# Kernel tuning notes

Hardware: AMD Instinct MI355X
Metric: run time of the kernel (lower is better)

The kernel has to match this reference:

```python
import jax, jax.numpy as jnp
import numpy as np

B, S, D = 2, 4096, 1024
H, HD = 16, 64
M = 512              # memseqlen == chunk size
L = 2 * M            # memory + chunk tokens
HID = 2816
EPS = 1e-5


def setup_inputs() -> dict:
    key = jax.random.key(0)
    ks = jax.random.split(key, 16)
    sc = 0.02
    return {
        "x": jax.random.normal(ks[0], (B, S, D), jnp.float32),
        "freqs_cos": jax.random.uniform(ks[1], (L, HD // 2), jnp.float32),
        "freqs_sin": jax.random.uniform(ks[2], (L, HD // 2), jnp.float32),
        "wq": jax.random.normal(ks[3], (D, D), jnp.float32) * sc,
        "wk": jax.random.normal(ks[4], (D, D), jnp.float32) * sc,
        "wv": jax.random.normal(ks[5], (D, D), jnp.float32) * sc,
        "wo": jax.random.normal(ks[6], (D, D), jnp.float32) * sc,
        "wm": jax.random.normal(ks[7], (D, D), jnp.float32) * sc,
        "wkm": jax.random.normal(ks[8], (D, D), jnp.float32) * sc,
        "wvm": jax.random.normal(ks[9], (D, D), jnp.float32) * sc,
        "w1": jax.random.normal(ks[10], (D, HID), jnp.float32) * sc,
        "w3": jax.random.normal(ks[11], (D, HID), jnp.float32) * sc,
        "w2": jax.random.normal(ks[12], (HID, D), jnp.float32) * sc,
        "ffn_norm_w": jnp.ones((D,), jnp.float32),
        "mem_norm_w": jnp.ones((D,), jnp.float32),
        "origin_mem": jnp.zeros((1, M, D), jnp.float32),
    }


def _rmsnorm(x, w):
    return x * jax.lax.rsqrt(jnp.mean(x * x, axis=-1, keepdims=True) + EPS) * w


def _rope(t, cos, sin):
    # t: (B, L, H, HD); cos/sin: (L, HD//2). Adjacent-pair complex rotation (llama2.c style).
    tr = t.reshape(*t.shape[:-1], HD // 2, 2)
    t_r, t_i = tr[..., 0], tr[..., 1]
    c = cos[None, :, None, :]
    s = sin[None, :, None, :]
    o_r = t_r * c - t_i * s
    o_i = t_r * s + t_i * c
    return jnp.stack([o_r, o_i], axis=-1).reshape(t.shape)


def reference(x, freqs_cos, freqs_sin, wq, wk, wv, wo, wm, wkm, wvm,
              w1, w2, w3, ffn_norm_w, mem_norm_w, origin_mem):
    bsz = x.shape[0]
    cos = freqs_cos[:L]
    sin = freqs_sin[:L]
    causal = jnp.tril(jnp.ones((L, L), dtype=bool))
    scale = 1.0 / jnp.sqrt(jnp.asarray(HD, x.dtype))

    def ffn(h):
        return (jax.nn.silu(h @ w1) * (h @ w3)) @ w2

    def step(om, subx):
        # token projections
        xq = (subx @ wq).reshape(bsz, M, H, HD)
        xk = (subx @ wk).reshape(bsz, M, H, HD)
        xv = (subx @ wv).reshape(bsz, M, H, HD)
        # memory glue: wm -> ffn residual -> rmsnorm
        om2 = om @ wm
        om2 = om2 + ffn(_rmsnorm(om2, ffn_norm_w))
        om2 = _rmsnorm(om2, mem_norm_w)
        # memory projections (source bug: mq is overwritten by mk; wqm unused)
        mk = (om2 @ wkm).reshape(bsz, M, H, HD)
        mv = (om2 @ wvm).reshape(bsz, M, H, HD)
        mq = mk
        q = jnp.concatenate([mq, xq], axis=1)  # (B, L, H, HD)
        k = jnp.concatenate([mk, xk], axis=1)
        v = jnp.concatenate([mv, xv], axis=1)
        q = _rope(q, cos, sin)
        k = _rope(k, cos, sin)
        # SDPA, causal over the concatenated length (n_rep == 1, repeat_kv is identity)
        qh = q.transpose(0, 2, 1, 3)
        kh = k.transpose(0, 2, 1, 3)
        vh = v.transpose(0, 2, 1, 3)
        scores = jnp.einsum('bhqd,bhkd->bhqk', qh, kh) * scale
        scores = jnp.where(causal, scores, jnp.finfo(scores.dtype).min)
        attn = jax.nn.softmax(scores, axis=-1)
        out = jnp.einsum('bhqk,bhkd->bhqd', attn, vh)
        out = out.transpose(0, 2, 1, 3).reshape(bsz, L, D)
        om_new = out[:, M:]  # token-part becomes next memory AND this chunk's output
        return om_new, om_new

    om0 = jnp.broadcast_to(origin_mem, (bsz, M, D))
    xc = x.reshape(bsz, S // M, M, D).transpose(1, 0, 2, 3)  # (n_chunks, B, M, D)
    _, outs = jax.lax.scan(step, om0, xc)
    out = outs.transpose(1, 0, 2, 3).reshape(bsz, S, D)
    return out @ wo
```

## Files before the change

kernel.cpp:

```cpp
#include <hip/hip_runtime.h>
#include <hip/hip_bf16.h>


#define D_    1024
#define H_    16
#define HD_   64
#define M_    512
#define L_    1024
#define HID_  2816
#define NSTEP 8

typedef __hip_bfloat16 bf16;
typedef _Float16 f16;
typedef __attribute__((ext_vector_type(8))) short short8;
typedef __attribute__((ext_vector_type(8))) _Float16 f16x8;
typedef __attribute__((ext_vector_type(2))) _Float16 f16x2;
typedef __attribute__((ext_vector_type(4))) float floatx4;

__global__ void probe_dtype(const void* x, int* flag) {
  int lane = threadIdx.x;
  unsigned short v = ((const unsigned short*)x)[2 * lane];
  int e = (v >> 7) & 0xFF;
  bool sane = (e >= 100 && e <= 140);
  unsigned long long m = __ballot(sane);
  if (lane == 0) flag[0] = (__popcll(m) >= 40) ? 1 : 0;
}

__device__ __forceinline__ float load_any(const void* p, long i, int isbf) {
  return isbf ? __bfloat162float(((const bf16*)p)[i]) : ((const float*)p)[i];
}

__global__ __launch_bounds__(256) void transpose_cast(const void* in, bf16* out,
                                                      int K, int N, const int* flagp) {
  __shared__ float tile[32][33];
  int isbf = flagp[0];
  int tx = threadIdx.x & 31, ty = threadIdx.x >> 5;
  int n = blockIdx.x * 32 + tx;
#pragma unroll
  for (int i = 0; i < 4; i++) {
    int k = blockIdx.y * 32 + ty + i * 8;
    tile[ty + i * 8][tx] = load_any(in, (long)k * N + n, isbf);
  }
  __syncthreads();
  int k2 = blockIdx.y * 32 + tx;
#pragma unroll
  for (int i = 0; i < 4; i++) {
    int n2 = blockIdx.x * 32 + ty + i * 8;
    out[(long)n2 * K + k2] = __float2bfloat16(tile[tx][ty + i * 8]);
  }
}

__global__ __launch_bounds__(256) void cast_to_bf16(const void* in, bf16* out, int n,
                                                    const int* flagp) {
  int i = blockIdx.x * 256 + threadIdx.x;
  if (i < n) out[i] = __float2bfloat16(load_any(in, i, flagp[0]));
}

__global__ __launch_bounds__(256) void cast_to_f32(const void* in, float* out, int n,
                                                   const int* flagp) {
  int i = blockIdx.x * 256 + threadIdx.x;
  if (i < n) out[i] = load_any(in, i, flagp[0]);
}

__global__ __launch_bounds__(256) void init_om(const void* in, bf16* om, const int* flagp) {
  int i = blockIdx.x * 256 + threadIdx.x;
  int rem = i & (M_ * D_ - 1);
  om[i] = __float2bfloat16(load_any(in, rem, flagp[0]));
}

__global__ __launch_bounds__(256) void gemm64(
    const bf16* __restrict__ A, const bf16* __restrict__ WT,
    void* __restrict__ out, const int* __restrict__ flagp,
    int N, int K, int out_mode) {
  __shared__ char smem[16384];
  char* aT = smem;
  char* bT = smem + 8192;
  int tid = threadIdx.x;
  int C0 = blockIdx.x * 64, R0 = blockIdx.y * 64;
  int wave = tid >> 6, lane = tid & 63;
  int wm_ = wave >> 1, wn_ = wave & 1;
  floatx4 acc[2][2] = {};

  int q0 = tid, q1 = tid + 256;
  int am0 = q0 >> 3, ac0 = q0 & 7;
  int am1 = q1 >> 3, ac1 = q1 & 7;
  long grow0 = R0 + am0, grow1 = R0 + am1;
  long bn0 = (long)(C0 + am0) * K, bn1 = (long)(C0 + am1) * K;
  int lofa0 = (am0 * 8 + (ac0 ^ (am0 & 7))) * 16;
  int lofa1 = (am1 * 8 + (ac1 ^ (am1 & 7))) * 16;

  for (int k0 = 0; k0 < K; k0 += 64) {
    uint4 va0 = *(const uint4*)(A + grow0 * K + k0 + ac0 * 8);
    uint4 va1 = *(const uint4*)(A + grow1 * K + k0 + ac1 * 8);
    uint4 vb0 = *(const uint4*)(WT + bn0 + k0 + ac0 * 8);
    uint4 vb1 = *(const uint4*)(WT + bn1 + k0 + ac1 * 8);
    __syncthreads();
    *(uint4*)(aT + lofa0) = va0;
    *(uint4*)(aT + lofa1) = va1;
    *(uint4*)(bT + lofa0) = vb0;
    *(uint4*)(bT + lofa1) = vb1;
    __syncthreads();
#pragma unroll
    for (int kki = 0; kki < 2; ++kki) {
      int cbase = kki * 4 + (lane >> 4);
      short8 af[2], bfr[2];
#pragma unroll
      for (int i = 0; i < 2; ++i) {
        int ml = wm_ * 32 + i * 16 + (lane & 15);
        af[i] = *(const short8*)(aT + (ml * 8 + (cbase ^ (ml & 7))) * 16);
        int nl = wn_ * 32 + i * 16 + (lane & 15);
        bfr[i] = *(const short8*)(bT + (nl * 8 + (cbase ^ (nl & 7))) * 16);
      }
#pragma unroll
      for (int i = 0; i < 2; ++i)
#pragma unroll
        for (int j = 0; j < 2; ++j)
          acc[i][j] = __builtin_amdgcn_mfma_f32_16x16x32_bf16(af[i], bfr[j], acc[i][j], 0, 0, 0);
    }
  }
  int isbf = flagp[0];
#pragma unroll
  for (int i = 0; i < 2; ++i)
#pragma unroll
    for (int j = 0; j < 2; ++j) {
      int row = R0 + wm_ * 32 + i * 16 + (lane >> 4) * 4;
      int col = C0 + wn_ * 32 + j * 16 + (lane & 15);
#pragma unroll
      for (int rg = 0; rg < 4; ++rg) {
        float v = acc[i][j][rg];
        long off = (long)(row + rg) * N + col;
        if (out_mode == 0) ((float*)out)[off] = v;
        else if (out_mode == 1) ((f16*)out)[off] = (f16)v;
        else {
          if (isbf) ((bf16*)out)[off] = __float2bfloat16(v);
          else ((float*)out)[off] = v;
        }
      }
    }
}

__global__ __launch_bounds__(256) void gemm128(
    const bf16* __restrict__ A, const bf16* __restrict__ WT,
    void* __restrict__ out, const int* __restrict__ flagp,
    int N, int K, int out_mode) {
  __shared__ char smem[32768];
  int tid = threadIdx.x;
  int w = tid >> 6, lane = tid & 63;
  int C0 = blockIdx.x * 128, R0 = blockIdx.y * 128;
  int wm = (w >> 1) * 64, wn = (w & 1) * 64;
  int g = lane >> 4, n16 = lane & 15;
  floatx4 acc[4][4] = {};
  int lr = lane >> 3, lc = lane & 7;

  for (int k0 = 0; k0 < K; k0 += 64) {
    __syncthreads();
#pragma unroll
    for (int i = 0; i < 4; ++i) {
      int m = w * 32 + i * 8 + lr;
      int cg = lc ^ (m & 7);
      const bf16* ga = A + (size_t)(R0 + m) * K + k0 + cg * 8;
      const bf16* gb = WT + (size_t)(C0 + m) * K + k0 + cg * 8;
      __builtin_amdgcn_global_load_lds(
          (const __attribute__((address_space(1))) void*)ga,
          (__attribute__((address_space(3))) void*)(smem + (w * 32 + i * 8) * 128),
          16, 0, 0);
      __builtin_amdgcn_global_load_lds(
          (const __attribute__((address_space(1))) void*)gb,
          (__attribute__((address_space(3))) void*)(smem + 16384 + (w * 32 + i * 8) * 128),
          16, 0, 0);
    }
    __syncthreads();
#pragma unroll
    for (int kk = 0; kk < 2; ++kk) {
      short8 af[4], bfr[4];
#pragma unroll
      for (int i = 0; i < 4; ++i) {
        int ml = wm + i * 16 + n16;
        af[i] = *(const short8*)(smem + (ml * 8 + ((kk * 4 + g) ^ (ml & 7))) * 16);
        int nl = wn + i * 16 + n16;
        bfr[i] = *(const short8*)(smem + 16384 + (nl * 8 + ((kk * 4 + g) ^ (nl & 7))) * 16);
      }
#pragma unroll
      for (int i = 0; i < 4; ++i)
#pragma unroll
        for (int j = 0; j < 4; ++j)
          acc[i][j] = __builtin_amdgcn_mfma_f32_16x16x32_bf16(af[i], bfr[j], acc[i][j], 0, 0, 0);
    }
  }
  int isbf = flagp[0];
#pragma unroll
  for (int i = 0; i < 4; ++i)
#pragma unroll
    for (int j = 0; j < 4; ++j) {
      int row = R0 + wm + i * 16 + g * 4;
      int col = C0 + wn + j * 16 + n16;
#pragma unroll
      for (int rg = 0; rg < 4; ++rg) {
        float v = acc[i][j][rg];
        long off = (long)(row + rg) * N + col;
        if (out_mode == 0) ((float*)out)[off] = v;
        else if (out_mode == 1) ((f16*)out)[off] = (f16)v;
        else {
          if (isbf) ((bf16*)out)[off] = __float2bfloat16(v);
          else ((float*)out)[off] = v;
        }
      }
    }
}

__global__ __launch_bounds__(256) void rmsnorm_cast(const float* __restrict__ X,
                                                    const float* __restrict__ Wn,
                                                    bf16* __restrict__ Y,
                                                    const float* __restrict__ Xadd) {
  int row = blockIdx.x, tid = threadIdx.x;
  const float* xr = X + (long)row * D_;
  float vals[4], ss = 0.f;
#pragma unroll
  for (int i = 0; i < 4; i++) {
    int c = tid + i * 256;
    float v = xr[c];
    if (Xadd) v += Xadd[(long)row * D_ + c];
    vals[i] = v;
    ss += v * v;
  }
#pragma unroll
  for (int off = 32; off; off >>= 1) ss += __shfl_xor(ss, off);
  __shared__ float wsum[4];
  int wv = tid >> 6, lane = tid & 63;
  if (lane == 0) wsum[wv] = ss;
  __syncthreads();
  ss = wsum[0] + wsum[1] + wsum[2] + wsum[3];
  float r = rsqrtf(ss * (1.0f / D_) + 1e-5f);
#pragma unroll
  for (int i = 0; i < 4; i++) {
    int c = tid + i * 256;
    Y[(long)row * D_ + c] = __float2bfloat16(vals[i] * r * Wn[c]);
  }
}

__global__ __launch_bounds__(256) void silu_mul_cast(const float* __restrict__ g13,
                                                     bf16* __restrict__ u) {
  int c = blockIdx.x * 256 + threadIdx.x;
  int r = blockIdx.y;
  float a = g13[(long)r * (2 * HID_) + c];
  float b = g13[(long)r * (2 * HID_) + HID_ + c];
  float s = a / (1.f + __expf(-a));
  u[(long)r * HID_ + c] = __float2bfloat16(s * b);
}

__global__ __launch_bounds__(256) void rope_x(
    const f16* __restrict__ qkv, const float* __restrict__ cosf,
    const float* __restrict__ sinf, f16* __restrict__ q_x,
    f16* __restrict__ k_x, f16* __restrict__ v_xT) {
  __shared__ f16 tile[64][72];
  int pt = blockIdx.x;
  int t = blockIdx.y;
  int bh = blockIdx.z;
  int b = bh >> 4, h = bh & 15;
  int tid = threadIdx.x;
  int i = tid & 31, p0 = tid >> 5;
  size_t slab = (size_t)t * 32 + bh;
#pragma unroll
  for (int j = 0; j < 8; ++j) {
    int pl = p0 + j * 8;
    int m = pt * 64 + pl;
    int pos = 512 + m;
    long base = ((long)b * 4096 + t * 512 + m) * 3072 + h * 64 + 2 * i;
    float c = cosf[pos * 32 + i], s = sinf[pos * 32 + i];
    float q0 = (float)qkv[base], q1 = (float)qkv[base + 1];
    f16x2 qw; qw.x = (f16)((q0 * c - q1 * s) * 0.125f);
    qw.y = (f16)((q0 * s + q1 * c) * 0.125f);
    *(f16x2*)(q_x + (slab * 512 + m) * 64 + 2 * i) = qw;
    float k0 = (float)qkv[base + 1024], k1 = (float)qkv[base + 1025];
    f16x2 kw; kw.x = (f16)(k0 * c - k1 * s); kw.y = (f16)(k0 * s + k1 * c);
    *(f16x2*)(k_x + (slab * 512 + m) * 64 + 2 * i) = kw;
    tile[2 * i][pl] = qkv[base + 2048];
    tile[2 * i + 1][pl] = qkv[base + 2049];
  }
  __syncthreads();
#pragma unroll
  for (int j = 0; j < 8; ++j) {
    int d = p0 + j * 8;
    f16x2 vv; vv.x = tile[d][2 * i]; vv.y = tile[d][2 * i + 1];
    *(f16x2*)(v_xT + (slab * 64 + d) * 512 + pt * 64 + 2 * i) = vv;
  }
}

__global__ __launch_bounds__(256) void rope_mem(
    const f16* __restrict__ mkv, const float* __restrict__ cosf,
    const float* __restrict__ sinf, f16* __restrict__ k_mem,
    f16* __restrict__ v_memT) {
  __shared__ f16 tile[64][72];
  int pt = blockIdx.x;
  int bh = blockIdx.y;
  int b = bh >> 4, h = bh & 15;
  int tid = threadIdx.x;
  int i = tid & 31, p0 = tid >> 5;
#pragma unroll
  for (int j = 0; j < 8; ++j) {
    int pl = p0 + j * 8;
    int pos = pt * 64 + pl;
    long base = ((long)(b * 512 + pos)) * 2048 + h * 64 + 2 * i;
    float c = cosf[pos * 32 + i], s = sinf[pos * 32 + i];
    float k0 = (float)mkv[base], k1 = (float)mkv[base + 1];
    f16x2 kw; kw.x = (f16)(k0 * c - k1 * s); kw.y = (f16)(k0 * s + k1 * c);
    *(f16x2*)(k_mem + ((size_t)bh * 512 + pos) * 64 + 2 * i) = kw;
    tile[2 * i][pl] = mkv[base + 1024];
    tile[2 * i + 1][pl] = mkv[base + 1025];
  }
  __syncthreads();
#pragma unroll
  for (int j = 0; j < 8; ++j) {
    int d = p0 + j * 8;
    f16x2 vv; vv.x = tile[d][2 * i]; vv.y = tile[d][2 * i + 1];
    *(f16x2*)(v_memT + ((size_t)bh * 64 + d) * 512 + pt * 64 + 2 * i) = vv;
  }
}

__global__ __launch_bounds__(256) void attn_mfma(
    const f16* __restrict__ q_x, const f16* __restrict__ k_mem,
    const f16* __restrict__ v_memT, const f16* __restrict__ k_x,
    const f16* __restrict__ v_xT, bf16* __restrict__ om_bf,
    bf16* __restrict__ outs_bf, int t) {
  __shared__ char smem[24576];
  int qt = blockIdx.x, bh = blockIdx.y;
  int tid = threadIdx.x;
  int w = tid >> 6, lane = tid & 63;
  int g = lane >> 4, n16 = lane & 15;
  int numc = 9 + qt;
  int pos = 512 + qt * 64 + w * 16 + n16;
  size_t slab = (size_t)t * 32 + bh;

  f16x8 qf[2];
  {
    const f16* qp = q_x + (slab * 512 + qt * 64 + w * 16 + n16) * 64 + g * 8;
    qf[0] = *(const f16x8*)(qp);
    qf[1] = *(const f16x8*)(qp + 32);
  }
  floatx4 O[4] = {};
  float mrun = -1e30f, lrun = 0.f;

  int id0 = tid, id1 = tid + 256;
  int r0 = id0 >> 3, c0 = id0 & 7;
  int r1 = id1 >> 3, c1 = id1 & 7;
  int lof0 = ((r0 << 3) | (c0 ^ (r0 & 7))) * 16;
  int lof1 = ((r1 << 3) | (c1 ^ (r1 & 7))) * 16;

  auto kaddr = [&](int c, int r) -> const f16* {
    return (c < 8) ? k_mem + ((size_t)bh * 512 + c * 64 + r) * 64
                   : k_x + (slab * 512 + (c - 8) * 64 + r) * 64;
  };
  auto vaddr = [&](int c, int d) -> const f16* {
    return (c < 8) ? v_memT + ((size_t)bh * 64 + d) * 512 + c * 64
                   : v_xT + (slab * 64 + d) * 512 + (c - 8) * 64;
  };

  uint4 kv0 = *(const uint4*)(kaddr(0, r0) + c0 * 8);
  uint4 kv1 = *(const uint4*)(kaddr(0, r1) + c1 * 8);
  uint4 vv0 = *(const uint4*)(vaddr(0, r0) + c0 * 8);
  uint4 vv1 = *(const uint4*)(vaddr(0, r1) + c1 * 8);

  char* Pw = smem + 16384 + w * 2048;

  for (int c = 0; c < numc; ++c) {
    __syncthreads();
    *(uint4*)(smem + lof0) = kv0;
    *(uint4*)(smem + lof1) = kv1;
    *(uint4*)(smem + 8192 + lof0) = vv0;
    *(uint4*)(smem + 8192 + lof1) = vv1;
    if (c + 1 < numc) {
      kv0 = *(const uint4*)(kaddr(c + 1, r0) + c0 * 8);
      kv1 = *(const uint4*)(kaddr(c + 1, r1) + c1 * 8);
      vv0 = *(const uint4*)(vaddr(c + 1, r0) + c0 * 8);
      vv1 = *(const uint4*)(vaddr(c + 1, r1) + c1 * 8);
    }
    __syncthreads();

    floatx4 S[4] = {};
#pragma unroll
    for (int kk = 0; kk < 2; ++kk) {
#pragma unroll
      for (int tn = 0; tn < 4; ++tn) {
        int row = tn * 16 + n16;
        f16x8 kf = *(const f16x8*)(smem + (((row << 3) | ((kk * 4 + g) ^ (row & 7))) * 16));
        S[tn] = __builtin_amdgcn_mfma_f32_16x16x32_f16(kf, qf[kk], S[tn], 0, 0, 0);
      }
    }
    if (c == numc - 1) {
      int kb = 512 + (c - 8) * 64;
#pragma unroll
      for (int tn = 0; tn < 4; ++tn)
#pragma unroll
        for (int r = 0; r < 4; ++r) {
          int key = kb + tn * 16 + g * 4 + r;
          if (key > pos) S[tn][r] = -1e30f;
        }
    }
    float smax = -1e30f;
#pragma unroll
    for (int tn = 0; tn < 4; ++tn)
#pragma unroll
      for (int r = 0; r < 4; ++r) smax = fmaxf(smax, S[tn][r]);
    smax = fmaxf(smax, __shfl_xor(smax, 16));
    smax = fmaxf(smax, __shfl_xor(smax, 32));
    float newm = fmaxf(mrun, smax);
    float corr = __expf(mrun - newm);
    mrun = newm;
    float lsum = 0.f;
    f16 pv[16];
#pragma unroll
    for (int tn = 0; tn < 4; ++tn)
#pragma unroll
      for (int r = 0; r < 4; ++r) {
        float p = __expf(S[tn][r] - newm);
        lsum += p;
        pv[tn * 4 + r] = (f16)p;
      }
    lsum += __shfl_xor(lsum, 16);
    lsum += __shfl_xor(lsum, 32);
    lrun = lrun * corr + lsum;
    float cr[4];
#pragma unroll
    for (int r = 0; r < 4; ++r) cr[r] = __shfl(corr, g * 4 + r);
#pragma unroll
    for (int dt = 0; dt < 4; ++dt)
#pragma unroll
      for (int r = 0; r < 4; ++r) O[dt][r] *= cr[r];
#pragma unroll
    for (int tn = 0; tn < 4; ++tn)
#pragma unroll
      for (int r = 0; r < 4; ++r) {
        int kap = tn * 16 + g * 4 + r;
        *(f16*)(Pw + (((n16 << 3) | ((kap >> 3) ^ (n16 & 7))) * 16 + (kap & 7) * 2)) =
            pv[tn * 4 + r];
      }
#pragma unroll
    for (int kk = 0; kk < 2; ++kk) {
      f16x8 pf = *(const f16x8*)(Pw + (((n16 << 3) | ((kk * 4 + g) ^ (n16 & 7))) * 16));
#pragma unroll
      for (int dt = 0; dt < 4; ++dt) {
        int row = dt * 16 + n16;
        f16x8 vf =
            *(const f16x8*)(smem + 8192 + (((row << 3) | ((kk * 4 + g) ^ (row & 7))) * 16));
        O[dt] = __builtin_amdgcn_mfma_f32_16x16x32_f16(pf, vf, O[dt], 0, 0, 0);
      }
    }
  }
  float rl = 1.0f / lrun;
  float rlr[4];
#pragma unroll
  for (int r = 0; r < 4; ++r) rlr[r] = __shfl(rl, g * 4 + r);
  int b = bh >> 4, h = bh & 15;
#pragma unroll
  for (int dt = 0; dt < 4; ++dt)
#pragma unroll
    for (int r = 0; r < 4; ++r) {
      int qq = qt * 64 + w * 16 + g * 4 + r;
      bf16 v = __float2bfloat16(O[dt][r] * rlr[r]);
      size_t col = h * 64 + dt * 16 + n16;
      om_bf[((size_t)(b * 512 + qq)) * 1024 + col] = v;
      outs_bf[((size_t)(b * 4096 + t * 512 + qq)) * 1024 + col] = v;
    }
}

extern "C" void kernel_launch(void* const* d_in, const int* in_sizes, int n_in,
                              void* d_out, int out_size, void* d_ws, size_t ws_size,
                              hipStream_t stream) {
  (void)in_sizes; (void)n_in; (void)out_size; (void)ws_size;
  const void* x   = d_in[0];
  const void* fc  = d_in[1];
  const void* fs  = d_in[2];
  const void* wq  = d_in[3];
  const void* wk  = d_in[4];
  const void* wv  = d_in[5];
  const void* wo  = d_in[6];
  const void* wm  = d_in[7];
  const void* wkm = d_in[8];
  const void* wvm = d_in[9];
  const void* w1  = d_in[10];
  const void* w3  = d_in[11];
  const void* w2  = d_in[12];
  const void* fnw = d_in[13];
  const void* mnw = d_in[14];
  const void* om0 = d_in[15];

  char* p = (char*)d_ws;
  auto alloc = [&](size_t bytes) -> char* {
    char* r = p;
    p += (bytes + 255) & ~(size_t)255;
    return r;
  };
  int*   flag    = (int*)alloc(256);
  bf16*  wqkvT   = (bf16*)alloc((size_t)3 * 1048576 * 2);
  bf16*  wmT     = (bf16*)alloc((size_t)1048576 * 2);
  bf16*  wkmvmT  = (bf16*)alloc((size_t)2 * 1048576 * 2);
  bf16*  w13T    = (bf16*)alloc((size_t)2 * 2883584 * 2);
  bf16*  w2T     = (bf16*)alloc((size_t)2883584 * 2);
  bf16*  woT     = (bf16*)alloc((size_t)1048576 * 2);
  bf16*  xb      = (bf16*)alloc((size_t)8388608 * 2);
  float* cosf    = (float*)alloc((size_t)32768 * 4);
  float* sinf    = (float*)alloc((size_t)32768 * 4);
  float* ffnw    = (float*)alloc((size_t)1024 * 4);
  float* memw    = (float*)alloc((size_t)1024 * 4);
  bf16*  om_bf   = (bf16*)alloc((size_t)1048576 * 2);
  bf16*  outs_bf = (bf16*)alloc((size_t)8388608 * 2);
  f16*   q_x     = (f16*)alloc((size_t)8 * 32 * 512 * 64 * 2);
  f16*   k_x     = (f16*)alloc((size_t)8 * 32 * 512 * 64 * 2);
  f16*   v_xT    = (f16*)alloc((size_t)8 * 32 * 512 * 64 * 2);
  char*  shr     = alloc((size_t)8192 * 3072 * 2);
  f16*   qkvf_all = (f16*)shr;
  char*  lp = shr;
  auto lalloc = [&](size_t bytes) -> char* {
    char* r = lp;
    lp += (bytes + 255) & ~(size_t)255;
    return r;
  };
  float* om2a   = (float*)lalloc((size_t)1048576 * 4);
  bf16*  h_bf   = (bf16*)lalloc((size_t)1048576 * 2);
  float* g13    = (float*)lalloc((size_t)5767168 * 4);
  bf16*  u_bf   = (bf16*)lalloc((size_t)2883584 * 2);
  float* fbuf   = (float*)lalloc((size_t)1048576 * 4);
  bf16*  om2_bf = (bf16*)lalloc((size_t)1048576 * 2);
  f16*   mkv    = (f16*)lalloc((size_t)2097152 * 2);
  f16*   k_mem  = (f16*)lalloc((size_t)1048576 * 2);
  f16*   v_memT = (f16*)lalloc((size_t)1048576 * 2);

  dim3 tb(256);
  probe_dtype<<<1, 64, 0, stream>>>(x, flag);

  transpose_cast<<<dim3(32, 32), tb, 0, stream>>>(wq, wqkvT, 1024, 1024, flag);
  transpose_cast<<<dim3(32, 32), tb, 0, stream>>>(wk, wqkvT + 1048576, 1024, 1024, flag);
  transpose_cast<<<dim3(32, 32), tb, 0, stream>>>(wv, wqkvT + 2 * 1048576, 1024, 1024, flag);
  transpose_cast<<<dim3(32, 32), tb, 0, stream>>>(wm, wmT, 1024, 1024, flag);
  transpose_cast<<<dim3(32, 32), tb, 0, stream>>>(wkm, wkmvmT, 1024, 1024, flag);
  transpose_cast<<<dim3(32, 32), tb, 0, stream>>>(wvm, wkmvmT + 1048576, 1024, 1024, flag);
  transpose_cast<<<dim3(88, 32), tb, 0, stream>>>(w1, w13T, 1024, 2816, flag);
  transpose_cast<<<dim3(88, 32), tb, 0, stream>>>(w3, w13T + 2883584, 1024, 2816, flag);
  transpose_cast<<<dim3(32, 88), tb, 0, stream>>>(w2, w2T, 2816, 1024, flag);
  transpose_cast<<<dim3(32, 32), tb, 0, stream>>>(wo, woT, 1024, 1024, flag);

  cast_to_bf16<<<32768, tb, 0, stream>>>(x, xb, 8388608, flag);
  cast_to_f32<<<128, tb, 0, stream>>>(fc, cosf, 32768, flag);
  cast_to_f32<<<128, tb, 0, stream>>>(fs, sinf, 32768, flag);
  cast_to_f32<<<4, tb, 0, stream>>>(fnw, ffnw, 1024, flag);
  cast_to_f32<<<4, tb, 0, stream>>>(mnw, memw, 1024, flag);
  init_om<<<4096, tb, 0, stream>>>(om0, om_bf, flag);

  gemm128<<<dim3(24, 64), tb, 0, stream>>>(xb, wqkvT, qkvf_all, flag, 3072, 1024, 1);
  rope_x<<<dim3(8, 8, 32), tb, 0, stream>>>(qkvf_all, cosf, sinf, q_x, k_x, v_xT);

  for (int t = 0; t < NSTEP; ++t) {
    gemm64<<<dim3(16, 16), tb, 0, stream>>>(om_bf, wmT, om2a, flag, 1024, 1024, 0);
    rmsnorm_cast<<<1024, tb, 0, stream>>>(om2a, ffnw, h_bf, nullptr);
    gemm128<<<dim3(44, 8), tb, 0, stream>>>(h_bf, w13T, g13, flag, 5632, 1024, 0);
    silu_mul_cast<<<dim3(11, 1024), tb, 0, stream>>>(g13, u_bf);
    gemm64<<<dim3(16, 16), tb, 0, stream>>>(u_bf, w2T, fbuf, flag, 1024, 2816, 0);
    rmsnorm_cast<<<1024, tb, 0, stream>>>(om2a, memw, om2_bf, fbuf);
    gemm64<<<dim3(32, 16), tb, 0, stream>>>(om2_bf, wkmvmT, mkv, flag, 2048, 1024, 1);
    rope_mem<<<dim3(8, 32), tb, 0, stream>>>(mkv, cosf, sinf, k_mem, v_memT);
    attn_mfma<<<dim3(8, 32), tb, 0, stream>>>(q_x, k_mem, v_memT, k_x, v_xT,
                                              om_bf, outs_bf, t);
  }
  gemm128<<<dim3(8, 64), tb, 0, stream>>>(outs_bf, woT, d_out, flag, 1024, 1024, 2);
}
```

Baseline: 1.270 ms.

## Fuse scan loop into one persistent kernel with grid barriers and folded norms

```diff
diff --git a/kernel.cpp b/kernel.cpp
--- a/kernel.cpp
+++ b/kernel.cpp
@@ -2,12 +2,6 @@
 #include <hip/hip_bf16.h>
 
 
-#define D_    1024
-#define H_    16
-#define HD_   64
-#define M_    512
-#define L_    1024
-#define HID_  2816
 #define NSTEP 8
 
 typedef __hip_bfloat16 bf16;
@@ -30,113 +24,56 @@
   return isbf ? __bfloat162float(((const bf16*)p)[i]) : ((const float*)p)[i];
 }
 
-__global__ __launch_bounds__(256) void transpose_cast(const void* in, bf16* out,
-                                                      int K, int N, const int* flagp) {
+struct TArg { const void* src; const void* scl; bf16* dst; int K, N, start; };
+struct TArgs { TArg a[10]; };
+
+__global__ __launch_bounds__(256) void transpose_all(TArgs ta, const int* flagp) {
   __shared__ float tile[32][33];
   int isbf = flagp[0];
+  int bid = blockIdx.x;
+  int z = 0;
+  while (z < 9 && bid >= ta.a[z + 1].start) ++z;
+  const TArg& e = ta.a[z];
+  int local = bid - e.start;
+  int tnx = e.N >> 5;
+  int bx = local % tnx, by = local / tnx;
   int tx = threadIdx.x & 31, ty = threadIdx.x >> 5;
-  int n = blockIdx.x * 32 + tx;
+  int n = bx * 32 + tx;
 #pragma unroll
   for (int i = 0; i < 4; i++) {
-    int k = blockIdx.y * 32 + ty + i * 8;
-    tile[ty + i * 8][tx] = load_any(in, (long)k * N + n, isbf);
+    int k = by * 32 + ty + i * 8;
+    tile[ty + i * 8][tx] = load_any(e.src, (long)k * e.N + n, isbf);
   }
   __syncthreads();
-  int k2 = blockIdx.y * 32 + tx;
+  int k2 = by * 32 + tx;
+  float s = e.scl ? load_any(e.scl, k2, isbf) : 1.f;
 #pragma unroll
   for (int i = 0; i < 4; i++) {
-    int n2 = blockIdx.x * 32 + ty + i * 8;
-    out[(long)n2 * K + k2] = __float2bfloat16(tile[tx][ty + i * 8]);
+    int n2 = bx * 32 + ty + i * 8;
+    e.dst[(long)n2 * e.K + k2] = __float2bfloat16(tile[tx][ty + i * 8] * s);
   }
 }
 
-__global__ __launch_bounds__(256) void cast_to_bf16(const void* in, bf16* out, int n,
-                                                    const int* flagp) {
-  int i = blockIdx.x * 256 + threadIdx.x;
-  if (i < n) out[i] = __float2bfloat16(load_any(in, i, flagp[0]));
-}
-
-__global__ __launch_bounds__(256) void cast_to_f32(const void* in, float* out, int n,
-                                                   const int* flagp) {
-  int i = blockIdx.x * 256 + threadIdx.x;
-  if (i < n) out[i] = load_any(in, i, flagp[0]);
-}
-
-__global__ __launch_bounds__(256) void init_om(const void* in, bf16* om, const int* flagp) {
-  int i = blockIdx.x * 256 + threadIdx.x;
-  int rem = i & (M_ * D_ - 1);
-  om[i] = __float2bfloat16(load_any(in, rem, flagp[0]));
-}
-
-__global__ __launch_bounds__(256) void gemm64(
-    const bf16* __restrict__ A, const bf16* __restrict__ WT,
-    void* __restrict__ out, const int* __restrict__ flagp,
-    int N, int K, int out_mode) {
-  __shared__ char smem[16384];
-  char* aT = smem;
-  char* bT = smem + 8192;
-  int tid = threadIdx.x;
-  int C0 = blockIdx.x * 64, R0 = blockIdx.y * 64;
-  int wave = tid >> 6, lane = tid & 63;
-  int wm_ = wave >> 1, wn_ = wave & 1;
-  floatx4 acc[2][2] = {};
-
-  int q0 = tid, q1 = tid + 256;
-  int am0 = q0 >> 3, ac0 = q0 & 7;
-  int am1 = q1 >> 3, ac1 = q1 & 7;
-  long grow0 = R0 + am0, grow1 = R0 + am1;
-  long bn0 = (long)(C0 + am0) * K, bn1 = (long)(C0 + am1) * K;
-  int lofa0 = (am0 * 8 + (ac0 ^ (am0 & 7))) * 16;
-  int lofa1 = (am1 * 8 + (ac1 ^ (am1 & 7))) * 16;
-
-  for (int k0 = 0; k0 < K; k0 += 64) {
-    uint4 va0 = *(const uint4*)(A + grow0 * K + k0 + ac0 * 8);
-    uint4 va1 = *(const uint4*)(A + grow1 * K + k0 + ac1 * 8);
-    uint4 vb0 = *(const uint4*)(WT + bn0 + k0 + ac0 * 8);
-    uint4 vb1 = *(const uint4*)(WT + bn1 + k0 + ac1 * 8);
-    __syncthreads();
-    *(uint4*)(aT + lofa0) = va0;
-    *(uint4*)(aT + lofa1) = va1;
-    *(uint4*)(bT + lofa0) = vb0;
-    *(uint4*)(bT + lofa1) = vb1;
-    __syncthreads();
-#pragma unroll
-    for (int kki = 0; kki < 2; ++kki) {
-      int cbase = kki * 4 + (lane >> 4);
-      short8 af[2], bfr[2];
-#pragma unroll
-      for (int i = 0; i < 2; ++i) {
-        int ml = wm_ * 32 + i * 16 + (lane & 15);
-        af[i] = *(const short8*)(aT + (ml * 8 + (cbase ^ (ml & 7))) * 16);
-        int nl = wn_ * 32 + i * 16 + (lane & 15);
-        bfr[i] = *(const short8*)(bT + (nl * 8 + (cbase ^ (nl & 7))) * 16);
-      }
-#pragma unroll
-      for (int i = 0; i < 2; ++i)
-#pragma unroll
-        for (int j = 0; j < 2; ++j)
-          acc[i][j] = __builtin_amdgcn_mfma_f32_16x16x32_bf16(af[i], bfr[j], acc[i][j], 0, 0, 0);
-    }
-  }
+__global__ __launch_bounds__(256) void prep(const void* x, const void* fc,
+                                            const void* fs, const void* om0,
+                                            bf16* xb, float* cosf, float* sinf,
+                                            bf16* om_bf, float* rs1, float* rs2,
+                                            int* bar, const int* flagp) {
+  long idx = (long)blockIdx.x * 256 + threadIdx.x;
   int isbf = flagp[0];
-#pragma unroll
-  for (int i = 0; i < 2; ++i)
-#pragma unroll
-    for (int j = 0; j < 2; ++j) {
-      int row = R0 + wm_ * 32 + i * 16 + (lane >> 4) * 4;
-      int col = C0 + wn_ * 32 + j * 16 + (lane & 15);
-#pragma unroll
-      for (int rg = 0; rg < 4; ++rg) {
-        float v = acc[i][j][rg];
-        long off = (long)(row + rg) * N + col;
-        if (out_mode == 0) ((float*)out)[off] = v;
-        else if (out_mode == 1) ((f16*)out)[off] = (f16)v;
-        else {
-          if (isbf) ((bf16*)out)[off] = __float2bfloat16(v);
-          else ((float*)out)[off] = v;
-        }
-      }
-    }
+  if (idx < 8388608) { xb[idx] = __float2bfloat16(load_any(x, idx, isbf)); return; }
+  long i = idx - 8388608;
+  if (i < 32768) { cosf[i] = load_any(fc, i, isbf); return; }
+  i -= 32768;
+  if (i < 32768) { sinf[i] = load_any(fs, i, isbf); return; }
+  i -= 32768;
+  if (i < 1048576) { om_bf[i] = __float2bfloat16(load_any(om0, i & 524287, isbf)); return; }
+  i -= 1048576;
+  if (i < 1024) { rs1[i] = 0.f; return; }
+  i -= 1024;
+  if (i < 1024) { rs2[i] = 0.f; return; }
+  i -= 1024;
+  if (i < 128) bar[i] = 0;
 }
 
 __global__ __launch_bounds__(256) void gemm128(
@@ -206,46 +143,6 @@
         }
       }
     }
-}
-
-__global__ __launch_bounds__(256) void rmsnorm_cast(const float* __restrict__ X,
-                                                    const float* __restrict__ Wn,
-                                                    bf16* __restrict__ Y,
-                                                    const float* __restrict__ Xadd) {
-  int row = blockIdx.x, tid = threadIdx.x;
-  const float* xr = X + (long)row * D_;
-  float vals[4], ss = 0.f;
-#pragma unroll
-  for (int i = 0; i < 4; i++) {
-    int c = tid + i * 256;
-    float v = xr[c];
-    if (Xadd) v += Xadd[(long)row * D_ + c];
-    vals[i] = v;
-    ss += v * v;
-  }
-#pragma unroll
-  for (int off = 32; off; off >>= 1) ss += __shfl_xor(ss, off);
-  __shared__ float wsum[4];
-  int wv = tid >> 6, lane = tid & 63;
-  if (lane == 0) wsum[wv] = ss;
-  __syncthreads();
-  ss = wsum[0] + wsum[1] + wsum[2] + wsum[3];
-  float r = rsqrtf(ss * (1.0f / D_) + 1e-5f);
-#pragma unroll
-  for (int i = 0; i < 4; i++) {
-    int c = tid + i * 256;
-    Y[(long)row * D_ + c] = __float2bfloat16(vals[i] * r * Wn[c]);
-  }
-}
-
-__global__ __launch_bounds__(256) void silu_mul_cast(const float* __restrict__ g13,
-                                                     bf16* __restrict__ u) {
-  int c = blockIdx.x * 256 + threadIdx.x;
-  int r = blockIdx.y;
-  float a = g13[(long)r * (2 * HID_) + c];
-  float b = g13[(long)r * (2 * HID_) + HID_ + c];
-  float s = a / (1.f + __expf(-a));
-  u[(long)r * HID_ + c] = __float2bfloat16(s * b);
 }
 
 __global__ __launch_bounds__(256) void rope_x(
@@ -286,181 +183,489 @@
   }
 }
 
-__global__ __launch_bounds__(256) void rope_mem(
-    const f16* __restrict__ mkv, const float* __restrict__ cosf,
-    const float* __restrict__ sinf, f16* __restrict__ k_mem,
-    f16* __restrict__ v_memT) {
-  __shared__ f16 tile[64][72];
-  int pt = blockIdx.x;
-  int bh = blockIdx.y;
-  int b = bh >> 4, h = bh & 15;
-  int tid = threadIdx.x;
-  int i = tid & 31, p0 = tid >> 5;
-#pragma unroll
-  for (int j = 0; j < 8; ++j) {
-    int pl = p0 + j * 8;
-    int pos = pt * 64 + pl;
-    long base = ((long)(b * 512 + pos)) * 2048 + h * 64 + 2 * i;
-    float c = cosf[pos * 32 + i], s = sinf[pos * 32 + i];
-    float k0 = (float)mkv[base], k1 = (float)mkv[base + 1];
-    f16x2 kw; kw.x = (f16)(k0 * c - k1 * s); kw.y = (f16)(k0 * s + k1 * c);
-    *(f16x2*)(k_mem + ((size_t)bh * 512 + pos) * 64 + 2 * i) = kw;
-    tile[2 * i][pl] = mkv[base + 1024];
-    tile[2 * i + 1][pl] = mkv[base + 1025];
+#define NBLK 256
+__device__ __forceinline__ void gbar(int* bar) {
+  __syncthreads();
+  if (threadIdx.x == 0) {
+    __threadfence();
+    int* cnt = bar;
+    int* gen = bar + 64;
+    int g = __hip_atomic_load(gen, __ATOMIC_RELAXED, __HIP_MEMORY_SCOPE_AGENT);
+    int old = __hip_atomic_fetch_add(cnt, 1, __ATOMIC_ACQ_REL, __HIP_MEMORY_SCOPE_AGENT);
+    if (old == NBLK - 1) {
+      __hip_atomic_store(cnt, 0, __ATOMIC_RELAXED, __HIP_MEMORY_SCOPE_AGENT);
+      __hip_atomic_fetch_add(gen, 1, __ATOMIC_ACQ_REL, __HIP_MEMORY_SCOPE_AGENT);
+    } else {
+      while (__hip_atomic_load(gen, __ATOMIC_ACQUIRE, __HIP_MEMORY_SCOPE_AGENT) == g)
+        __builtin_amdgcn_s_sleep(2);
+    }
+    __threadfence();
   }
   __syncthreads();
-#pragma unroll
-  for (int j = 0; j < 8; ++j) {
-    int d = p0 + j * 8;
-    f16x2 vv; vv.x = tile[d][2 * i]; vv.y = tile[d][2 * i + 1];
-    *(f16x2*)(v_memT + ((size_t)bh * 64 + d) * 512 + pt * 64 + 2 * i) = vv;
-  }
-}
-
-__global__ __launch_bounds__(256) void attn_mfma(
-    const f16* __restrict__ q_x, const f16* __restrict__ k_mem,
-    const f16* __restrict__ v_memT, const f16* __restrict__ k_x,
-    const f16* __restrict__ v_xT, bf16* __restrict__ om_bf,
-    bf16* __restrict__ outs_bf, int t) {
-  __shared__ char smem[24576];
-  int qt = blockIdx.x, bh = blockIdx.y;
-  int tid = threadIdx.x;
+}
+
+__global__ __launch_bounds__(256) void scan_loop(
+    const bf16* __restrict__ wmT, const bf16* __restrict__ w13T,
+    const bf16* __restrict__ w2T, const bf16* __restrict__ wkmvmT,
+    const f16* __restrict__ q_x, const f16* __restrict__ k_x,
+    const f16* __restrict__ v_xT, const float* __restrict__ cosf,
+    const float* __restrict__ sinf, bf16* __restrict__ om_bf,
+    bf16* __restrict__ outs_bf, float* __restrict__ om2a,
+    float* __restrict__ g13, float* __restrict__ om2b,
+    f16* __restrict__ mkv, float* __restrict__ rs1, float* __restrict__ rs2,
+    int* __restrict__ bar) {
+  __shared__ char smem[32768];
+  int bid = blockIdx.x, tid = threadIdx.x;
   int w = tid >> 6, lane = tid & 63;
   int g = lane >> 4, n16 = lane & 15;
-  int numc = 9 + qt;
-  int pos = 512 + qt * 64 + w * 16 + n16;
-  size_t slab = (size_t)t * 32 + bh;
-
-  f16x8 qf[2];
-  {
-    const f16* qp = q_x + (slab * 512 + qt * 64 + w * 16 + n16) * 64 + g * 8;
-    qf[0] = *(const f16x8*)(qp);
-    qf[1] = *(const f16x8*)(qp + 32);
+  int wm_ = w >> 1, wn_ = w & 1;
+
+  for (int t = 0; t < NSTEP; ++t) {
+    {
+      int C0 = (bid & 15) * 64, R0 = (bid >> 4) * 64;
+      floatx4 acc[2][2] = {};
+      int am0 = tid >> 3, ac0 = tid & 7;
+      int am1 = (tid + 256) >> 3, ac1 = tid & 7;
+      long grow0 = R0 + am0, grow1 = R0 + am1;
+      long bn0 = (long)(C0 + am0) * 1024, bn1 = (long)(C0 + am1) * 1024;
+      int lofa0 = (am0 * 8 + (ac0 ^ (am0 & 7))) * 16;
+      int lofa1 = (am1 * 8 + (ac1 ^ (am1 & 7))) * 16;
+      for (int k0 = 0; k0 < 1024; k0 += 64) {
+        uint4 va0 = *(const uint4*)(om_bf + grow0 * 1024 + k0 + ac0 * 8);
+        uint4 va1 = *(const uint4*)(om_bf + grow1 * 1024 + k0 + ac1 * 8);
+        uint4 vb0 = *(const uint4*)(wmT + bn0 + k0 + ac0 * 8);
+        uint4 vb1 = *(const uint4*)(wmT + bn1 + k0 + ac1 * 8);
+        __syncthreads();
+        *(uint4*)(smem + lofa0) = va0;
+        *(uint4*)(smem + lofa1) = va1;
+        *(uint4*)(smem + 8192 + lofa0) = vb0;
+        *(uint4*)(smem + 8192 + lofa1) = vb1;
+        __syncthreads();
+#pragma unroll
+        for (int kki = 0; kki < 2; ++kki) {
+          int cb = kki * 4 + g;
+          short8 af[2], bfr[2];
+#pragma unroll
+          for (int i = 0; i < 2; ++i) {
+            int ml = wm_ * 32 + i * 16 + n16;
+            af[i] = *(const short8*)(smem + (ml * 8 + (cb ^ (ml & 7))) * 16);
+            int nl = wn_ * 32 + i * 16 + n16;
+            bfr[i] = *(const short8*)(smem + 8192 + (nl * 8 + (cb ^ (nl & 7))) * 16);
+          }
+#pragma unroll
+          for (int i = 0; i < 2; ++i)
+#pragma unroll
+            for (int j = 0; j < 2; ++j)
+              acc[i][j] = __builtin_amdgcn_mfma_f32_16x16x32_bf16(af[i], bfr[j], acc[i][j], 0, 0, 0);
+        }
+      }
+      __syncthreads();
+      float* rsl = (float*)(smem + 16384);
+      if (tid < 64) rsl[tid] = 0.f;
+      __syncthreads();
+#pragma unroll
+      for (int i = 0; i < 2; ++i)
+#pragma unroll
+        for (int rg = 0; rg < 4; ++rg) {
+          int rl = wm_ * 32 + i * 16 + g * 4 + rg;
+          float sq = 0.f;
+#pragma unroll
+          for (int j = 0; j < 2; ++j) {
+            float v = acc[i][j][rg];
+            sq += v * v;
+            om2a[(long)(R0 + rl) * 1024 + C0 + wn_ * 32 + j * 16 + n16] = v;
+          }
+          atomicAdd(&rsl[rl], sq);
+        }
+      __syncthreads();
+      if (tid < 64) atomicAdd(&rs1[R0 + tid], rsl[tid]);
+    }
+    gbar(bar);
+
+    for (int tile = bid; tile < 352; tile += NBLK) {
+      int C0 = (tile % 44) * 128, R0 = (tile / 44) * 128;
+      int wmm = (w >> 1) * 64, wnn = (w & 1) * 64;
+      floatx4 acc[4][4] = {};
+      int lr = lane >> 3, lc = lane & 7;
+      int ams[4], acs[4];
+      float sca[4];
+#pragma unroll
+      for (int i = 0; i < 4; ++i) {
+        int id = tid + 256 * i;
+        ams[i] = id >> 3;
+        acs[i] = id & 7;
+        sca[i] = rsqrtf(rs1[R0 + ams[i]] * (1.f / 1024.f) + 1e-5f);
+      }
+      for (int k0 = 0; k0 < 1024; k0 += 64) {
+        uint4 av[4];
+#pragma unroll
+        for (int i = 0; i < 4; ++i) {
+          const float* ap = om2a + (size_t)(R0 + ams[i]) * 1024 + k0 + acs[i] * 8;
+          float4 x0 = *(const float4*)ap, x1 = *(const float4*)(ap + 4);
+          union { bf16 b[8]; uint4 u; } pk;
+          pk.b[0] = __float2bfloat16(x0.x * sca[i]);
+          pk.b[1] = __float2bfloat16(x0.y * sca[i]);
+          pk.b[2] = __float2bfloat16(x0.z * sca[i]);
+          pk.b[3] = __float2bfloat16(x0.w * sca[i]);
+          pk.b[4] = __float2bfloat16(x1.x * sca[i]);
+          pk.b[5] = __float2bfloat16(x1.y * sca[i]);
+          pk.b[6] = __float2bfloat16(x1.z * sca[i]);
+          pk.b[7] = __float2bfloat16(x1.w * sca[i]);
+          av[i] = pk.u;
+        }
+        __syncthreads();
+#pragma unroll
+        for (int i = 0; i < 4; ++i)
+          *(uint4*)(smem + (ams[i] * 8 + (acs[i] ^ (ams[i] & 7))) * 16) = av[i];
+#pragma unroll
+        for (int i = 0; i < 4; ++i) {
+          int m = w * 32 + i * 8 + lr;
+          int cg = lc ^ (m & 7);
+          const bf16* gb = w13T + (size_t)(C0 + m) * 1024 + k0 + cg * 8;
+          __builtin_amdgcn_global_load_lds(
+              (const __attribute__((address_space(1))) void*)gb,
+              (__attribute__((address_space(3))) void*)(smem + 16384 + (w * 32 + i * 8) * 128),
+              16, 0, 0);
+        }
+        __syncthreads();
+#pragma unroll
+        for (int kk = 0; kk < 2; ++kk) {
+          short8 af[4], bfr[4];
+#pragma unroll
+          for (int i = 0; i < 4; ++i) {
+            int ml = wmm + i * 16 + n16;
+            af[i] = *(const short8*)(smem + (ml * 8 + ((kk * 4 + g) ^ (ml & 7))) * 16);
+            int nl = wnn + i * 16 + n16;
+            bfr[i] = *(const short8*)(smem + 16384 + (nl * 8 + ((kk * 4 + g) ^ (nl & 7))) * 16);
+          }
+#pragma unroll
+          for (int i = 0; i < 4; ++i)
+#pragma unroll
+            for (int j = 0; j < 4; ++j)
+              acc[i][j] = __builtin_amdgcn_mfma_f32_16x16x32_bf16(af[i], bfr[j], acc[i][j], 0, 0, 0);
+        }
+      }
+#pragma unroll
+      for (int i = 0; i < 4; ++i)
+#pragma unroll
+        for (int j = 0; j < 4; ++j) {
+          int row = R0 + wmm + i * 16 + g * 4;
+          int col = C0 + wnn + j * 16 + n16;
+#pragma unroll
+          for (int rg = 0; rg < 4; ++rg)
+            g13[(long)(row + rg) * 5632 + col] = acc[i][j][rg];
+        }
+      __syncthreads();
+    }
+    gbar(bar);
+
+    {
+      int C0 = (bid & 15) * 64, R0 = (bid >> 4) * 64;
+      floatx4 acc[2][2] = {};
+      int am0 = tid >> 3, ac0 = tid & 7;
+      int am1 = (tid + 256) >> 3, ac1 = tid & 7;
+      long bn0 = (long)(C0 + am0) * 2816, bn1 = (long)(C0 + am1) * 2816;
+      int lofa0 = (am0 * 8 + (ac0 ^ (am0 & 7))) * 16;
+      int lofa1 = (am1 * 8 + (ac1 ^ (am1 & 7))) * 16;
+      for (int k0 = 0; k0 < 2816; k0 += 64) {
+        uint4 va[2];
+        int amv[2] = {am0, am1}, acv[2] = {ac0, ac1};
+#pragma unroll
+        for (int i = 0; i < 2; ++i) {
+          const float* g1p = g13 + (size_t)(R0 + amv[i]) * 5632 + k0 + acv[i] * 8;
+          const float* g3p = g1p + 2816;
+          float4 a0 = *(const float4*)g1p, a1 = *(const float4*)(g1p + 4);
+          float4 b0 = *(const float4*)g3p, b1 = *(const float4*)(g3p + 4);
+          union { bf16 b[8]; uint4 u; } pk;
+          pk.b[0] = __float2bfloat16(a0.x / (1.f + __expf(-a0.x)) * b0.x);
+          pk.b[1] = __float2bfloat16(a0.y / (1.f + __expf(-a0.y)) * b0.y);
+          pk.b[2] = __float2bfloat16(a0.z / (1.f + __expf(-a0.z)) * b0.z);
+          pk.b[3] = __float2bfloat16(a0.w / (1.f + __expf(-a0.w)) * b0.w);
+          pk.b[4] = __float2bfloat16(a1.x / (1.f + __expf(-a1.x)) * b1.x);
+          pk.b[5] = __float2bfloat16(a1.y / (1.f + __expf(-a1.y)) * b1.y);
+          pk.b[6] = __float2bfloat16(a1.z / (1.f + __expf(-a1.z)) * b1.z);
+          pk.b[7] = __float2bfloat16(a1.w / (1.f + __expf(-a1.w)) * b1.w);
+          va[i] = pk.u;
+        }
+        uint4 vb0 = *(const uint4*)(w2T + bn0 + k0 + ac0 * 8);
+        uint4 vb1 = *(const uint4*)(w2T + bn1 + k0 + ac1 * 8);
+        __syncthreads();
+        *(uint4*)(smem + lofa0) = va[0];
+        *(uint4*)(smem + lofa1) = va[1];
+        *(uint4*)(smem + 8192 + lofa0) = vb0;
+        *(uint4*)(smem + 8192 + lofa1) = vb1;
+        __syncthreads();
+#pragma unroll
+        for (int kki = 0; kki < 2; ++kki) {
+          int cb = kki * 4 + g;
+          short8 af[2], bfr[2];
+#pragma unroll
+          for (int i = 0; i < 2; ++i) {
+            int ml = wm_ * 32 + i * 16 + n16;
+            af[i] = *(const short8*)(smem + (ml * 8 + (cb ^ (ml & 7))) * 16);
+            int nl = wn_ * 32 + i * 16 + n16;
+            bfr[i] = *(const short8*)(smem + 8192 + (nl * 8 + (cb ^ (nl & 7))) * 16);
+          }
+#pragma unroll
+          for (int i = 0; i < 2; ++i)
+#pragma unroll
+            for (int j = 0; j < 2; ++j)
+              acc[i][j] = __builtin_amdgcn_mfma_f32_16x16x32_bf16(af[i], bfr[j], acc[i][j], 0, 0, 0);
+        }
+      }
+      __syncthreads();
+      float* rsl = (float*)(smem + 16384);
+      if (tid < 64) rsl[tid] = 0.f;
+      __syncthreads();
+#pragma unroll
+      for (int i = 0; i < 2; ++i)
+#pragma unroll
+        for (int rg = 0; rg < 4; ++rg) {
+          int rl = wm_ * 32 + i * 16 + g * 4 + rg;
+          float sq = 0.f;
+#pragma unroll
+          for (int j = 0; j < 2; ++j) {
+            long off = (long)(R0 + rl) * 1024 + C0 + wn_ * 32 + j * 16 + n16;
+            float o2 = om2a[off] + acc[i][j][rg];
+            om2b[off] = o2;
+            sq += o2 * o2;
+          }
+          atomicAdd(&rsl[rl], sq);
+        }
+      __syncthreads();
+      if (tid < 64) atomicAdd(&rs2[R0 + tid], rsl[tid]);
+    }
+    gbar(bar);
+
+#pragma unroll
+    for (int half = 0; half < 2; ++half) {
+      int tile = bid + half * NBLK;
+      int C0 = (tile & 31) * 64, R0 = (tile >> 5) * 64;
+      floatx4 acc[2][2] = {};
+      int am0 = tid >> 3, ac0 = tid & 7;
+      int am1 = (tid + 256) >> 3, ac1 = tid & 7;
+      long bn0 = (long)(C0 + am0) * 1024, bn1 = (long)(C0 + am1) * 1024;
+      int lofa0 = (am0 * 8 + (ac0 ^ (am0 & 7))) * 16;
+      int lofa1 = (am1 * 8 + (ac1 ^ (am1 & 7))) * 16;
+      float sc0 = rsqrtf(rs2[R0 + am0] * (1.f / 1024.f) + 1e-5f);
+      float sc1 = rsqrtf(rs2[R0 + am1] * (1.f / 1024.f) + 1e-5f);
+      for (int k0 = 0; k0 < 1024; k0 += 64) {
+        uint4 va[2];
+        int amv[2] = {am0, am1}, acv[2] = {ac0, ac1};
+        float scv[2] = {sc0, sc1};
+#pragma unroll
+        for (int i = 0; i < 2; ++i) {
+          const float* ap = om2b + (size_t)(R0 + amv[i]) * 1024 + k0 + acv[i] * 8;
+          float4 x0 = *(const float4*)ap, x1 = *(const float4*)(ap + 4);
+          union { bf16 b[8]; uint4 u; } pk;
+          pk.b[0] = __float2bfloat16(x0.x * scv[i]);
+          pk.b[1] = __float2bfloat16(x0.y * scv[i]);
+          pk.b[2] = __float2bfloat16(x0.z * scv[i]);
+          pk.b[3] = __float2bfloat16(x0.w * scv[i]);
+          pk.b[4] = __float2bfloat16(x1.x * scv[i]);
+          pk.b[5] = __float2bfloat16(x1.y * scv[i]);
+          pk.b[6] = __float2bfloat16(x1.z * scv[i]);
+          pk.b[7] = __float2bfloat16(x1.w * scv[i]);
+          va[i] = pk.u;
+        }
+        uint4 vb0 = *(const uint4*)(wkmvmT + bn0 + k0 + ac0 * 8);
+        uint4 vb1 = *(const uint4*)(wkmvmT + bn1 + k0 + ac1 * 8);
+        __syncthreads();
+        *(uint4*)(smem + lofa0) = va[0];
+        *(uint4*)(smem + lofa1) = va[1];
+        *(uint4*)(smem + 8192 + lofa0) = vb0;
+        *(uint4*)(smem + 8192 + lofa1) = vb1;
+        __syncthreads();
+#pragma unroll
+        for (int kki = 0; kki < 2; ++kki) {
+          int cb = kki * 4 + g;
+          short8 af[2], bfr[2];
+#pragma unroll
+          for (int i = 0; i < 2; ++i) {
+            int ml = wm_ * 32 + i * 16 + n16;
+            af[i] = *(const short8*)(smem + (ml * 8 + (cb ^ (ml & 7))) * 16);
+            int nl = wn_ * 32 + i * 16 + n16;
+            bfr[i] = *(const short8*)(smem + 8192 + (nl * 8 + (cb ^ (nl & 7))) * 16);
+          }
+#pragma unroll
+          for (int i = 0; i < 2; ++i)
+#pragma unroll
+            for (int j = 0; j < 2; ++j)
+              acc[i][j] = __builtin_amdgcn_mfma_f32_16x16x32_bf16(af[i], bfr[j], acc[i][j], 0, 0, 0);
+        }
+      }
+#pragma unroll
+      for (int i = 0; i < 2; ++i)
+#pragma unroll
+        for (int j = 0; j < 2; ++j) {
+          int row = R0 + wm_ * 32 + i * 16 + g * 4;
+          int col = C0 + wn_ * 32 + j * 16 + n16;
+#pragma unroll
+          for (int rg = 0; rg < 4; ++rg)
+            mkv[(long)(row + rg) * 2048 + col] = (f16)acc[i][j][rg];
+        }
+      __syncthreads();
+    }
+    gbar(bar);
+
+    {
+      if (bid == 0) {
+        rs1[tid] = 0.f; rs1[tid + 256] = 0.f; rs1[tid + 512] = 0.f; rs1[tid + 768] = 0.f;
+      } else if (bid == 1) {
+        rs2[tid] = 0.f; rs2[tid + 256] = 0.f; rs2[tid + 512] = 0.f; rs2[tid + 768] = 0.f;
+      }
+      int qt = bid & 7, bh = bid >> 3;
+      int batb = bh >> 4, hh = bh & 15;
+      int numc = 9 + qt;
+      int pos = 512 + qt * 64 + w * 16 + n16;
+      size_t slab = (size_t)t * 32 + bh;
+      f16x8 qf[2];
+      {
+        const f16* qp = q_x + (slab * 512 + qt * 64 + w * 16 + n16) * 64 + g * 8;
+        qf[0] = *(const f16x8*)(qp);
+        qf[1] = *(const f16x8*)(qp + 32);
+      }
+      floatx4 O[4] = {};
+      float mrun = -1e30f, lrun = 0.f;
+      int r0 = tid >> 3, c0 = tid & 7;
+      int r1 = (tid + 256) >> 3, c1 = tid & 7;
+      int lof0 = ((r0 << 3) | (c0 ^ (r0 & 7))) * 16;
+      int lof1 = ((r1 << 3) | (c1 ^ (r1 & 7))) * 16;
+
+      auto ld_k = [&](int c, int r, int dc) -> uint4 {
+        union { f16x8 h; uint4 u; } cv;
+        if (c < 8) {
+          int pp = c * 64 + r;
+          f16x8 kv = *(const f16x8*)(mkv + ((size_t)(batb * 512 + pp)) * 2048 + hh * 64 + dc * 8);
+#pragma unroll
+          for (int j = 0; j < 4; ++j) {
+            float cs = cosf[pp * 32 + dc * 4 + j], sn = sinf[pp * 32 + dc * 4 + j];
+            float a = (float)kv[2 * j], bq = (float)kv[2 * j + 1];
+            cv.h[2 * j] = (f16)(a * cs - bq * sn);
+            cv.h[2 * j + 1] = (f16)(a * sn + bq * cs);
+          }
+        } else {
+          cv.u = *(const uint4*)(k_x + (slab * 512 + (c - 8) * 64 + r) * 64 + dc * 8);
+        }
+        return cv.u;
+      };
+      auto ld_v = [&](int c, int r, int dc) -> uint4 {
+        union { f16x8 h; uint4 u; } cv;
+        if (c < 8) {
+#pragma unroll
+          for (int j = 0; j < 8; ++j)
+            cv.h[j] = mkv[((size_t)(batb * 512 + c * 64 + dc * 8 + j)) * 2048 + 1024 + hh * 64 + r];
+        } else {
+          cv.u = *(const uint4*)(v_xT + (slab * 64 + r) * 512 + (c - 8) * 64 + dc * 8);
+        }
+        return cv.u;
+      };
+
+      uint4 kv0 = ld_k(0, r0, c0), kv1 = ld_k(0, r1, c1);
+      uint4 vv0 = ld_v(0, r0, c0), vv1 = ld_v(0, r1, c1);
+      char* Pw = smem + 16384 + w * 2048;
+
+      for (int c = 0; c < numc; ++c) {
+        __syncthreads();
+        *(uint4*)(smem + lof0) = kv0;
+        *(uint4*)(smem + lof1) = kv1;
+        *(uint4*)(smem + 8192 + lof0) = vv0;
+        *(uint4*)(smem + 8192 + lof1) = vv1;
+        if (c + 1 < numc) {
+          kv0 = ld_k(c + 1, r0, c0);
+          kv1 = ld_k(c + 1, r1, c1);
+          vv0 = ld_v(c + 1, r0, c0);
+          vv1 = ld_v(c + 1, r1, c1);
+        }
+        __syncthreads();
+
+        floatx4 S[4] = {};
+#pragma unroll
+        for (int kk = 0; kk < 2; ++kk) {
+#pragma unroll
+          for (int tn = 0; tn < 4; ++tn) {
+            int row = tn * 16 + n16;
+            f16x8 kf = *(const f16x8*)(smem + (((row << 3) | ((kk * 4 + g) ^ (row & 7))) * 16));
+            S[tn] = __builtin_amdgcn_mfma_f32_16x16x32_f16(kf, qf[kk], S[tn], 0, 0, 0);
+          }
+        }
+        if (c == numc - 1) {
+          int kb = 512 + (c - 8) * 64;
+#pragma unroll
+          for (int tn = 0; tn < 4; ++tn)
+#pragma unroll
+            for (int r = 0; r < 4; ++r) {
+              int key = kb + tn * 16 + g * 4 + r;
+              if (key > pos) S[tn][r] = -1e30f;
+            }
+        }
+        float smax = -1e30f;
+#pragma unroll
+        for (int tn = 0; tn < 4; ++tn)
+#pragma unroll
+          for (int r = 0; r < 4; ++r) smax = fmaxf(smax, S[tn][r]);
+        smax = fmaxf(smax, __shfl_xor(smax, 16));
+        smax = fmaxf(smax, __shfl_xor(smax, 32));
+        float newm = fmaxf(mrun, smax);
+        float corr = __expf(mrun - newm);
+        mrun = newm;
+        float lsum = 0.f;
+        f16 pv[16];
+#pragma unroll
+        for (int tn = 0; tn < 4; ++tn)
+#pragma unroll
+          for (int r = 0; r < 4; ++r) {
+            float p = __expf(S[tn][r] - newm);
+            lsum += p;
+            pv[tn * 4 + r] = (f16)p;
+          }
+        lsum += __shfl_xor(lsum, 16);
+        lsum += __shfl_xor(lsum, 32);
+        lrun = lrun * corr + lsum;
+        float cr[4];
+#pragma unroll
+        for (int r = 0; r < 4; ++r) cr[r] = __shfl(corr, g * 4 + r);
+#pragma unroll
+        for (int dt = 0; dt < 4; ++dt)
+#pragma unroll
+          for (int r = 0; r < 4; ++r) O[dt][r] *= cr[r];
+#pragma unroll
+        for (int tn = 0; tn < 4; ++tn)
+#pragma unroll
+          for (int r = 0; r < 4; ++r) {
+            int kap = tn * 16 + g * 4 + r;
+            *(f16*)(Pw + (((n16 << 3) | ((kap >> 3) ^ (n16 & 7))) * 16 + (kap & 7) * 2)) =
+                pv[tn * 4 + r];
+          }
+#pragma unroll
+        for (int kk = 0; kk < 2; ++kk) {
+          f16x8 pf = *(const f16x8*)(Pw + (((n16 << 3) | ((kk * 4 + g) ^ (n16 & 7))) * 16));
+#pragma unroll
+          for (int dt = 0; dt < 4; ++dt) {
+            int row = dt * 16 + n16;
+            f16x8 vf =
+                *(const f16x8*)(smem + 8192 + (((row << 3) | ((kk * 4 + g) ^ (row & 7))) * 16));
+            O[dt] = __builtin_amdgcn_mfma_f32_16x16x32_f16(pf, vf, O[dt], 0, 0, 0);
+          }
+        }
+      }
+      float rl = 1.0f / lrun;
+      float rlr[4];
+#pragma unroll
+      for (int r = 0; r < 4; ++r) rlr[r] = __shfl(rl, g * 4 + r);
+#pragma unroll
+      for (int dt = 0; dt < 4; ++dt)
+#pragma unroll
+        for (int r = 0; r < 4; ++r) {
+          int qq = qt * 64 + w * 16 + g * 4 + r;
+          bf16 v = __float2bfloat16(O[dt][r] * rlr[r]);
+          size_t col = hh * 64 + dt * 16 + n16;
+          om_bf[((size_t)(batb * 512 + qq)) * 1024 + col] = v;
+          outs_bf[((size_t)(batb * 4096 + t * 512 + qq)) * 1024 + col] = v;
+        }
+    }
+    gbar(bar);
   }
-  floatx4 O[4] = {};
-  float mrun = -1e30f, lrun = 0.f;
-
-  int id0 = tid, id1 = tid + 256;
-  int r0 = id0 >> 3, c0 = id0 & 7;
-  int r1 = id1 >> 3, c1 = id1 & 7;
-  int lof0 = ((r0 << 3) | (c0 ^ (r0 & 7))) * 16;
-  int lof1 = ((r1 << 3) | (c1 ^ (r1 & 7))) * 16;
-
-  auto kaddr = [&](int c, int r) -> const f16* {
-    return (c < 8) ? k_mem + ((size_t)bh * 512 + c * 64 + r) * 64
-                   : k_x + (slab * 512 + (c - 8) * 64 + r) * 64;
-  };
-  auto vaddr = [&](int c, int d) -> const f16* {
-    return (c < 8) ? v_memT + ((size_t)bh * 64 + d) * 512 + c * 64
-                   : v_xT + (slab * 64 + d) * 512 + (c - 8) * 64;
-  };
-
-  uint4 kv0 = *(const uint4*)(kaddr(0, r0) + c0 * 8);
-  uint4 kv1 = *(const uint4*)(kaddr(0, r1) + c1 * 8);
-  uint4 vv0 = *(const uint4*)(vaddr(0, r0) + c0 * 8);
-  uint4 vv1 = *(const uint4*)(vaddr(0, r1) + c1 * 8);
-
-  char* Pw = smem + 16384 + w * 2048;
-
-  for (int c = 0; c < numc; ++c) {
-    __syncthreads();
-    *(uint4*)(smem + lof0) = kv0;
-    *(uint4*)(smem + lof1) = kv1;
-    *(uint4*)(smem + 8192 + lof0) = vv0;
-    *(uint4*)(smem + 8192 + lof1) = vv1;
-    if (c + 1 < numc) {
-      kv0 = *(const uint4*)(kaddr(c + 1, r0) + c0 * 8);
-      kv1 = *(const uint4*)(kaddr(c + 1, r1) + c1 * 8);
-      vv0 = *(const uint4*)(vaddr(c + 1, r0) + c0 * 8);
-      vv1 = *(const uint4*)(vaddr(c + 1, r1) + c1 * 8);
-    }
-    __syncthreads();
-
-    floatx4 S[4] = {};
-#pragma unroll
-    for (int kk = 0; kk < 2; ++kk) {
-#pragma unroll
-      for (int tn = 0; tn < 4; ++tn) {
-        int row = tn * 16 + n16;
-        f16x8 kf = *(const f16x8*)(smem + (((row << 3) | ((kk * 4 + g) ^ (row & 7))) * 16));
-        S[tn] = __builtin_amdgcn_mfma_f32_16x16x32_f16(kf, qf[kk], S[tn], 0, 0, 0);
-      }
-    }
-    if (c == numc - 1) {
-      int kb = 512 + (c - 8) * 64;
-#pragma unroll
-      for (int tn = 0; tn < 4; ++tn)
-#pragma unroll
-        for (int r = 0; r < 4; ++r) {
-          int key = kb + tn * 16 + g * 4 + r;
-          if (key > pos) S[tn][r] = -1e30f;
-        }
-    }
-    float smax = -1e30f;
-#pragma unroll
-    for (int tn = 0; tn < 4; ++tn)
-#pragma unroll
-      for (int r = 0; r < 4; ++r) smax = fmaxf(smax, S[tn][r]);
-    smax = fmaxf(smax, __shfl_xor(smax, 16));
-    smax = fmaxf(smax, __shfl_xor(smax, 32));
-    float newm = fmaxf(mrun, smax);
-    float corr = __expf(mrun - newm);
-    mrun = newm;
-    float lsum = 0.f;
-    f16 pv[16];
-#pragma unroll
-    for (int tn = 0; tn < 4; ++tn)
-#pragma unroll
-      for (int r = 0; r < 4; ++r) {
-        float p = __expf(S[tn][r] - newm);
-        lsum += p;
-        pv[tn * 4 + r] = (f16)p;
-      }
-    lsum += __shfl_xor(lsum, 16);
-    lsum += __shfl_xor(lsum, 32);
-    lrun = lrun * corr + lsum;
-    float cr[4];
-#pragma unroll
-    for (int r = 0; r < 4; ++r) cr[r] = __shfl(corr, g * 4 + r);
-#pragma unroll
-    for (int dt = 0; dt < 4; ++dt)
-#pragma unroll
-      for (int r = 0; r < 4; ++r) O[dt][r] *= cr[r];
-#pragma unroll
-    for (int tn = 0; tn < 4; ++tn)
-#pragma unroll
-      for (int r = 0; r < 4; ++r) {
-        int kap = tn * 16 + g * 4 + r;
-        *(f16*)(Pw + (((n16 << 3) | ((kap >> 3) ^ (n16 & 7))) * 16 + (kap & 7) * 2)) =
-            pv[tn * 4 + r];
-      }
-#pragma unroll
-    for (int kk = 0; kk < 2; ++kk) {
-      f16x8 pf = *(const f16x8*)(Pw + (((n16 << 3) | ((kk * 4 + g) ^ (n16 & 7))) * 16));
-#pragma unroll
-      for (int dt = 0; dt < 4; ++dt) {
-        int row = dt * 16 + n16;
-        f16x8 vf =
-            *(const f16x8*)(smem + 8192 + (((row << 3) | ((kk * 4 + g) ^ (row & 7))) * 16));
-        O[dt] = __builtin_amdgcn_mfma_f32_16x16x32_f16(pf, vf, O[dt], 0, 0, 0);
-      }
-    }
-  }
-  float rl = 1.0f / lrun;
-  float rlr[4];
-#pragma unroll
-  for (int r = 0; r < 4; ++r) rlr[r] = __shfl(rl, g * 4 + r);
-  int b = bh >> 4, h = bh & 15;
-#pragma unroll
-  for (int dt = 0; dt < 4; ++dt)
-#pragma unroll
-    for (int r = 0; r < 4; ++r) {
-      int qq = qt * 64 + w * 16 + g * 4 + r;
-      bf16 v = __float2bfloat16(O[dt][r] * rlr[r]);
-      size_t col = h * 64 + dt * 16 + n16;
-      om_bf[((size_t)(b * 512 + qq)) * 1024 + col] = v;
-      outs_bf[((size_t)(b * 4096 + t * 512 + qq)) * 1024 + col] = v;
-    }
 }
 
 extern "C" void kernel_launch(void* const* d_in, const int* in_sizes, int n_in,
@@ -491,6 +696,7 @@
     return r;
   };
   int*   flag    = (int*)alloc(256);
+  int*   bar     = (int*)alloc(512);
   bf16*  wqkvT   = (bf16*)alloc((size_t)3 * 1048576 * 2);
   bf16*  wmT     = (bf16*)alloc((size_t)1048576 * 2);
   bf16*  wkmvmT  = (bf16*)alloc((size_t)2 * 1048576 * 2);
@@ -500,13 +706,13 @@
   bf16*  xb      = (bf16*)alloc((size_t)8388608 * 2);
   float* cosf    = (float*)alloc((size_t)32768 * 4);
   float* sinf    = (float*)alloc((size_t)32768 * 4);
-  float* ffnw    = (float*)alloc((size_t)1024 * 4);
-  float* memw    = (float*)alloc((size_t)1024 * 4);
   bf16*  om_bf   = (bf16*)alloc((size_t)1048576 * 2);
   bf16*  outs_bf = (bf16*)alloc((size_t)8388608 * 2);
   f16*   q_x     = (f16*)alloc((size_t)8 * 32 * 512 * 64 * 2);
   f16*   k_x     = (f16*)alloc((size_t)8 * 32 * 512 * 64 * 2);
   f16*   v_xT    = (f16*)alloc((size_t)8 * 32 * 512 * 64 * 2);
+  float* rs1     = (float*)alloc((size_t)1024 * 4);
+  float* rs2     = (float*)alloc((size_t)1024 * 4);
   char*  shr     = alloc((size_t)8192 * 3072 * 2);
   f16*   qkvf_all = (f16*)shr;
   char*  lp = shr;
@@ -515,51 +721,42 @@
     lp += (bytes + 255) & ~(size_t)255;
     return r;
   };
-  float* om2a   = (float*)lalloc((size_t)1048576 * 4);
-  bf16*  h_bf   = (bf16*)lalloc((size_t)1048576 * 2);
-  float* g13    = (float*)lalloc((size_t)5767168 * 4);
-  bf16*  u_bf   = (bf16*)lalloc((size_t)2883584 * 2);
-  float* fbuf   = (float*)lalloc((size_t)1048576 * 4);
-  bf16*  om2_bf = (bf16*)lalloc((size_t)1048576 * 2);
-  f16*   mkv    = (f16*)lalloc((size_t)2097152 * 2);
-  f16*   k_mem  = (f16*)lalloc((size_t)1048576 * 2);
-  f16*   v_memT = (f16*)lalloc((size_t)1048576 * 2);
+  float* om2a = (float*)lalloc((size_t)1048576 * 4);
+  float* g13  = (float*)lalloc((size_t)5767168 * 4);
+  float* om2b = (float*)lalloc((size_t)1048576 * 4);
+  f16*   mkv  = (f16*)lalloc((size_t)2097152 * 2);
 
   dim3 tb(256);
   probe_dtype<<<1, 64, 0, stream>>>(x, flag);
 
-  transpose_cast<<<dim3(32, 32), tb, 0, stream>>>(wq, wqkvT, 1024, 1024, flag);
-  transpose_cast<<<dim3(32, 32), tb, 0, stream>>>(wk, wqkvT + 1048576, 1024, 1024, flag);
-  transpose_cast<<<dim3(32, 32), tb, 0, stream>>>(wv, wqkvT + 2 * 1048576, 1024, 1024, flag);
-  transpose_cast<<<dim3(32, 32), tb, 0, stream>>>(wm, wmT, 1024, 1024, flag);
-  transpose_cast<<<dim3(32, 32), tb, 0, stream>>>(wkm, wkmvmT, 1024, 1024, flag);
-  transpose_cast<<<dim3(32, 32), tb, 0, stream>>>(wvm, wkmvmT + 1048576, 1024, 1024, flag);
-  transpose_cast<<<dim3(88, 32), tb, 0, stream>>>(w1, w13T, 1024, 2816, flag);
-  transpose_cast<<<dim3(88, 32), tb, 0, stream>>>(w3, w13T + 2883584, 1024, 2816, flag);
-  transpose_cast<<<dim3(32, 88), tb, 0, stream>>>(w2, w2T, 2816, 1024, flag);
-  transpose_cast<<<dim3(32, 32), tb, 0, stream>>>(wo, woT, 1024, 1024, flag);
-
-  cast_to_bf16<<<32768, tb, 0, stream>>>(x, xb, 8388608, flag);
-  cast_to_f32<<<128, tb, 0, stream>>>(fc, cosf, 32768, flag);
-  cast_to_f32<<<128, tb, 0, stream>>>(fs, sinf, 32768, flag);
-  cast_to_f32<<<4, tb, 0, stream>>>(fnw, ffnw, 1024, flag);
-  cast_to_f32<<<4, tb, 0, stream>>>(mnw, memw, 1024, flag);
-  init_om<<<4096, tb, 0, stream>>>(om0, om_bf, flag);
+  TArgs ta;
+  int start = 0;
+  auto addT = [&](int i, const void* src, const void* scl, bf16* dst, int K, int N) {
+    ta.a[i].src = src; ta.a[i].scl = scl; ta.a[i].dst = dst;
+    ta.a[i].K = K; ta.a[i].N = N; ta.a[i].start = start;
+    start += (N / 32) * (K / 32);
+  };
+  addT(0, wq, nullptr, wqkvT, 1024, 1024);
+  addT(1, wk, nullptr, wqkvT + 1048576, 1024, 1024);
+  addT(2, wv, nullptr, wqkvT + 2 * 1048576, 1024, 1024);
+  addT(3, wm, nullptr, wmT, 1024, 1024);
+  addT(4, wkm, mnw, wkmvmT, 1024, 1024);
+  addT(5, wvm, mnw, wkmvmT + 1048576, 1024, 1024);
+  addT(6, w1, fnw, w13T, 1024, 2816);
+  addT(7, w3, fnw, w13T + 2816 * 1024, 1024, 2816);
+  addT(8, w2, nullptr, w2T, 2816, 1024);
+  addT(9, wo, nullptr, woT, 1024, 1024);
+  transpose_all<<<start, tb, 0, stream>>>(ta, flag);
+
+  prep<<<37129, tb, 0, stream>>>(x, fc, fs, om0, xb, cosf, sinf, om_bf, rs1, rs2,
+                                 bar, flag);
 
   gemm128<<<dim3(24, 64), tb, 0, stream>>>(xb, wqkvT, qkvf_all, flag, 3072, 1024, 1);
   rope_x<<<dim3(8, 8, 32), tb, 0, stream>>>(qkvf_all, cosf, sinf, q_x, k_x, v_xT);
 
-  for (int t = 0; t < NSTEP; ++t) {
-    gemm64<<<dim3(16, 16), tb, 0, stream>>>(om_bf, wmT, om2a, flag, 1024, 1024, 0);
-    rmsnorm_cast<<<1024, tb, 0, stream>>>(om2a, ffnw, h_bf, nullptr);
-    gemm128<<<dim3(44, 8), tb, 0, stream>>>(h_bf, w13T, g13, flag, 5632, 1024, 0);
-    silu_mul_cast<<<dim3(11, 1024), tb, 0, stream>>>(g13, u_bf);
-    gemm64<<<dim3(16, 16), tb, 0, stream>>>(u_bf, w2T, fbuf, flag, 1024, 2816, 0);
-    rmsnorm_cast<<<1024, tb, 0, stream>>>(om2a, memw, om2_bf, fbuf);
-    gemm64<<<dim3(32, 16), tb, 0, stream>>>(om2_bf, wkmvmT, mkv, flag, 2048, 1024, 1);
-    rope_mem<<<dim3(8, 32), tb, 0, stream>>>(mkv, cosf, sinf, k_mem, v_memT);
-    attn_mfma<<<dim3(8, 32), tb, 0, stream>>>(q_x, k_mem, v_memT, k_x, v_xT,
-                                              om_bf, outs_bf, t);
-  }
+  scan_loop<<<dim3(NBLK), tb, 0, stream>>>(wmT, w13T, w2T, wkmvmT, q_x, k_x, v_xT,
+                                           cosf, sinf, om_bf, outs_bf, om2a, g13,
+                                           om2b, mkv, rs1, rs2, bar);
+
   gemm128<<<dim3(8, 64), tb, 0, stream>>>(outs_bf, woT, d_out, flag, 1024, 1024, 2);
 }
```

Result: slower. 3.346 ms (+163.4%).
